# Kernel tuning notes

Measured on AMD Instinct MI355X. Metric: run time of the kernel, lower is better.

The kernel has to match this reference:

```python
import jax, jax.numpy as jnp
import numpy as np

B, N = 2, 6
C_IN, C_MID = 512, 512
D, C_OUT = 112, 80
OGH, OGW, DS = 256, 704, 16
FH, FW = OGH // DS, OGW // DS  # 16, 44
D_MIN, D_MAX = 2.0, 58.0
NX, NY, NZ = 128, 128, 1
VSIZE = np.array([0.8, 0.8, 8.0], dtype=np.float32)
VCOORD = np.array([-51.2 + 0.4, -51.2 + 0.4, -5.0 + 4.0], dtype=np.float32)


def make_frustum():
    # (D, FH, FW, 4) with entries (x_pix, y_pix, depth, 1)
    ones = jnp.ones((D, FH, FW), jnp.float32)
    d = jnp.linspace(D_MIN, D_MAX, D)[:, None, None] * jnp.ones((1, FH, FW))
    x = jnp.linspace(0.0, OGW - 1.0, FW)[None, None, :] * jnp.ones((D, FH, 1))
    y = jnp.linspace(0.0, OGH - 1.0, FH)[None, :, None] * jnp.ones((D, 1, FW))
    return jnp.stack([x, y, d, ones], axis=-1)


def setup_inputs() -> dict:
    key = jax.random.key(0)
    ks = jax.random.split(key, 24)
    eye = jnp.eye(4, dtype=jnp.float32)
    K = jnp.array([[1266.0, 0.0, 800.0, 0.0],
                   [0.0, 1266.0, 450.0, 0.0],
                   [0.0, 0.0, 1.0, 0.0],
                   [0.0, 0.0, 0.0, 1.0]], jnp.float32)
    inp = {
        'feat': jax.random.normal(ks[0], (B * N, C_IN, FH, FW), jnp.float32),
        'w1': 0.05 * jax.random.normal(ks[1], (C_MID, C_IN, 3, 3), jnp.float32),
        'g1': 1.0 + 0.1 * jax.random.normal(ks[2], (C_MID,), jnp.float32),
        'b1': 0.1 * jax.random.normal(ks[3], (C_MID,), jnp.float32),
        'm1': 0.1 * jax.random.normal(ks[4], (C_MID,), jnp.float32),
        'v1': 0.5 + jax.random.uniform(ks[5], (C_MID,), jnp.float32),
        'w2': 0.05 * jax.random.normal(ks[6], (C_MID, C_MID, 3, 3), jnp.float32),
        'g2': 1.0 + 0.1 * jax.random.normal(ks[7], (C_MID,), jnp.float32),
        'b2': 0.1 * jax.random.normal(ks[8], (C_MID,), jnp.float32),
        'm2': 0.1 * jax.random.normal(ks[9], (C_MID,), jnp.float32),
        'v2': 0.5 + jax.random.uniform(ks[10], (C_MID,), jnp.float32),
        'w_out': 0.05 * jax.random.normal(ks[11], (D + C_OUT, C_MID, 1, 1), jnp.float32),
        'b_out': 0.1 * jax.random.normal(ks[12], (D + C_OUT,), jnp.float32),
        'sensor2ego': eye + 0.05 * jax.random.normal(ks[13], (B, N, 4, 4), jnp.float32),
        'sensor2virtual': eye + 0.05 * jax.random.normal(ks[14], (B, N, 4, 4), jnp.float32),
        'intrin': K + 0.01 * jax.random.normal(ks[15], (B, N, 4, 4), jnp.float32),
        'ida': eye + 0.01 * jax.random.normal(ks[16], (B, N, 4, 4), jnp.float32),
        'ref_heights': 1.5 + 0.2 * jax.random.normal(ks[17], (B, N), jnp.float32),
        'bda': eye + 0.01 * jax.random.normal(ks[18], (B, 4, 4), jnp.float32),
    }
    return inp


def _conv(x, w, p):
    return jax.lax.conv_general_dilated(x, w, (1, 1), [(p, p), (p, p)],
                                         dimension_numbers=('NCHW', 'OIHW', 'NCHW'))


def _bn(x, g, b, m, v):
    s = (g / jnp.sqrt(v + 1e-5))
    return (x - m[None, :, None, None]) * s[None, :, None, None] + b[None, :, None, None]


def get_geometry(sensor2ego, sensor2virtual, intrin, ida, ref_heights, bda):
    frustum = make_frustum()[..., None]  # (D,FH,FW,4,1)
    pts = jnp.linalg.inv(ida)[:, :, None, None, None] @ frustum  # (B,N,D,FH,FW,4,1)
    ref = ref_heights[:, :, None, None, None, None]
    height = -pts[..., 2, :] + ref  # (B,N,D,FH,FW,1)
    pc = pts.at[..., 2, :].set(10.0)
    pc = jnp.concatenate([pc[..., :2, :] * pc[..., 2:3, :], pc[..., 2:, :]], axis=-2)
    cv = sensor2virtual @ jnp.linalg.inv(intrin)
    pv = cv[:, :, None, None, None] @ pc
    ratio = height[..., 0] / pv[..., 1, 0]  # (B,N,D,FH,FW)
    pts = pv * ratio[..., None, None]
    pts = pts.at[..., 3, :].set(1.0)
    ce = sensor2ego @ jnp.linalg.inv(sensor2virtual)
    pts = ce[:, :, None, None, None] @ pts
    pts = (bda[:, None, None, None, None] @ pts)[..., 0]
    return pts[..., :3]  # (B,N,D,FH,FW,3)


def reference(feat, w1, g1, b1, m1, v1, w2, g2, b2, m2, v2, w_out, b_out,
              sensor2ego, sensor2virtual, intrin, ida, ref_heights, bda):
    # DepthNet head
    h = jax.nn.relu(_bn(_conv(feat, w1, 1), g1, b1, m1, v1))
    h = jax.nn.relu(_bn(_conv(h, w2, 1), g2, b2, m2, v2))
    hf = _conv(h, w_out, 0) + b_out[None, :, None, None]  # (B*N, D+C, FH, FW)
    depth = jax.nn.softmax(hf[:, :D], axis=1).reshape(B, N, D, FH, FW)
    context = hf[:, D:].reshape(B, N, C_OUT, FH, FW)

    geom = get_geometry(sensor2ego, sensor2virtual, intrin, ida, ref_heights, bda)

    # voxel indices
    vsize = jnp.asarray(VSIZE)
    vcoord = jnp.asarray(VCOORD)
    idx = ((geom - (vcoord - vsize / 2.0)) / vsize).astype(jnp.int32)
    valid = (jnp.all(idx >= 0, axis=-1) & (idx[..., 0] < NX)
             & (idx[..., 1] < NY) & (idx[..., 2] < NZ))

    # LSS outer product: (B,N,D,FH,FW,C)
    vol = jnp.einsum('bndhw,bnchw->bndhwc', depth, context)
    YX = NY * NX
    sid = idx[..., 1] * NX + idx[..., 0] + jnp.arange(B, dtype=jnp.int32)[:, None, None, None, None] * YX
    sid = jnp.where(valid, sid, B * YX).reshape(-1)
    bev = jax.ops.segment_sum(vol.reshape(-1, C_OUT), sid, num_segments=B * YX + 1)[:B * YX]
    return bev.reshape(B, NY, NX, C_OUT).transpose(0, 3, 1, 2)  # (B,C,NY,NX)
```

## Files before the change

### kernel.cpp

```cpp
#include <hip/hip_runtime.h>
#include <stdint.h>

#define NB   2
#define NN   6
#define NIMG 12
#define CIN  512
#define CMID 512
#define DD   112
#define COUT 80
#define FHh  16
#define FWw  44
#define NPIX 704
#define NPOS 8448
#define KK   4608
#define NXg  128
#define NYg  128
#define YX   16384
#define MAT_STRIDE 56
#define PADPIX 828
#define PROW 46
#define KSPLIT 4
#define KCHUNK (KK/KSPLIT)

typedef short short8 __attribute__((ext_vector_type(8)));
typedef float f32x4  __attribute__((ext_vector_type(4)));

#define GLD16(g, l) __builtin_amdgcn_global_load_lds((const __attribute__((address_space(1))) void*)(g), (__attribute__((address_space(3))) void*)(l), 16, 0, 0)

__device__ __forceinline__ unsigned short f2bf(float f){
  unsigned u = __float_as_uint(f);
  u += 0x7fffu + ((u >> 16) & 1u);
  return (unsigned short)(u >> 16);
}

__device__ __forceinline__ f32x4 mfma16(short8 a, short8 b, f32x4 c){
  return __builtin_amdgcn_mfma_f32_16x16x32_bf16(a, b, c, 0, 0, 0);
}

__global__ void k_f32_to_bf16(const float* __restrict__ src, unsigned short* __restrict__ dst, int n){
  for (int i = blockIdx.x*blockDim.x + threadIdx.x; i < n; i += gridDim.x*blockDim.x)
    dst[i] = f2bf(src[i]);
}

__global__ void k_wreorder(const float* __restrict__ src, unsigned short* __restrict__ dst){
  int i = blockIdx.x*blockDim.x + threadIdx.x;
  int oc = i / KK; int j = i - oc*KK;
  int r = j >> 9; int ic = j & 511;
  dst[i] = f2bf(src[(size_t)(oc*512 + ic)*9 + r]);
}

__global__ void k_bn_prep(const float* __restrict__ g, const float* __restrict__ b,
                          const float* __restrict__ m, const float* __restrict__ v,
                          float* __restrict__ scale, float* __restrict__ bias){
  int t = blockIdx.x*blockDim.x + threadIdx.x;
  if (t < CMID){
    float s = g[t] / sqrtf(v[t] + 1e-5f);
    scale[t] = s;
    bias[t]  = b[t] - m[t]*s;
  }
}

__global__ void k_featpad(const float* __restrict__ feat, unsigned short* __restrict__ dst){
  int blk = blockIdx.x;
  int img = blk >> 4, y = blk & 15;
  const float* s = feat + (size_t)img*CIN*NPIX + y*FWw;
  unsigned short* d = dst + (size_t)img*PADPIX*512 + ((y+1)*PROW + 1)*512;
  for (int j = threadIdx.x; j < FWw*512; j += 256){
    int x = j >> 9, ic = j & 511;
    d[x*512 + ic] = f2bf(s[(size_t)ic*NPIX + x]);
  }
}

__device__ void inv4(const double* A, double* out){
  double M[4][8];
  for (int i=0;i<4;i++){ for(int j=0;j<4;j++){ M[i][j]=A[i*4+j]; M[i][4+j]=(i==j)?1.0:0.0; } }
  for (int c=0;c<4;c++){
    int piv=c; double best=fabs(M[c][c]);
    for (int r=c+1;r<4;r++){ double a=fabs(M[r][c]); if(a>best){best=a;piv=r;} }
    if (piv!=c){ for(int j=0;j<8;j++){ double tt=M[c][j]; M[c][j]=M[piv][j]; M[piv][j]=tt; } }
    double inv = 1.0 / M[c][c];
    for (int j=0;j<8;j++) M[c][j]*=inv;
    for (int r=0;r<4;r++){ if(r==c) continue; double f=M[r][c];
      for (int j=0;j<8;j++) M[r][j]-=f*M[c][j]; }
  }
  for (int i=0;i<4;i++) for(int j=0;j<4;j++) out[i*4+j]=M[i][4+j];
}
__device__ void mm4(const double* A, const double* Bm, double* C){
  for (int i=0;i<4;i++) for(int j=0;j<4;j++){
    double s=0.0; for(int k=0;k<4;k++) s+=A[i*4+k]*Bm[k*4+j]; C[i*4+j]=s; }
}

__global__ void k_prep_mats(const float* __restrict__ s2e, const float* __restrict__ s2v,
                            const float* __restrict__ intr, const float* __restrict__ ida,
                            const float* __restrict__ refh, const float* __restrict__ bda,
                            double* __restrict__ mats){
  int t = threadIdx.x;
  if (t >= NIMG) return;
  int b = t / NN;
  double Mida[16], Ms2v[16], Mintr[16], Ms2e[16], Mbda[16];
  for (int i=0;i<16;i++){
    Mida[i] =(double)ida [t*16+i];
    Ms2v[i] =(double)s2v [t*16+i];
    Mintr[i]=(double)intr[t*16+i];
    Ms2e[i] =(double)s2e [t*16+i];
    Mbda[i] =(double)bda [b*16+i];
  }
  double* o = mats + (size_t)t*MAT_STRIDE;
  double tmp[16], tmp2[16];
  inv4(Mida, o);
  inv4(Mintr, tmp);  mm4(Ms2v, tmp, o+16);
  inv4(Ms2v, tmp);   mm4(Ms2e, tmp, tmp2);
  mm4(Mbda, tmp2, o+32);
  o[48] = (double)refh[t];
}

__global__ void k_geom(const double* __restrict__ mats, int* __restrict__ sid){
  int g = blockIdx.x*blockDim.x + threadIdx.x;
  int img = g / (DD*NPIX); int rem = g - img*(DD*NPIX);
  int d = rem / NPIX; int p = rem - d*NPIX;
  int h = p / FWw; int w = p - h*FWw;
  const double* M = mats + (size_t)img*MAT_STRIDE;
  float xf = (float)w * (703.0f/43.0f);
  float yf = (float)h * 17.0f;
  float df = 2.0f + (float)d * (56.0f/111.0f);
  double x = (double)xf, y = (double)yf, dep = (double)df;
  double p0 = M[0]*x + M[1]*y + M[2]*dep + M[3];
  double p1 = M[4]*x + M[5]*y + M[6]*dep + M[7];
  double p2 = M[8]*x + M[9]*y + M[10]*dep + M[11];
  double p3 = M[12]*x + M[13]*y + M[14]*dep + M[15];
  double height = M[48] - p2;
  double c0 = p0*10.0, c1 = p1*10.0, c2 = 10.0, c3 = p3;
  const double* C = M + 16;
  double q0 = C[0]*c0 + C[1]*c1 + C[2]*c2 + C[3]*c3;
  double q1 = C[4]*c0 + C[5]*c1 + C[6]*c2 + C[7]*c3;
  double q2 = C[8]*c0 + C[9]*c1 + C[10]*c2 + C[11]*c3;
  double ratio = height / q1;
  double r0 = q0*ratio, r1 = q1*ratio, r2 = q2*ratio, r3 = 1.0;
  const double* F = M + 32;
  double gx = F[0]*r0 + F[1]*r1 + F[2]*r2 + F[3]*r3;
  double gy = F[4]*r0 + F[5]*r1 + F[6]*r2 + F[7]*r3;
  double gz = F[8]*r0 + F[9]*r1 + F[10]*r2 + F[11]*r3;
  float gxf = (float)gx, gyf = (float)gy, gzf = (float)gz;
  const float vcx = (float)(-51.2 + 0.4);
  const float ox = vcx - 0.4f;
  const float oy = ox;
  const float oz = -1.0f - 4.0f;
  float tx = (gxf - ox) / 0.8f;
  float ty = (gyf - oy) / 0.8f;
  float tz = (gzf - oz) / 8.0f;
  int ix = (int)tx, iy = (int)ty, iz = (int)tz;
  bool valid = (tx==tx) && (ty==ty) && (tz==tz) &&
               (ix >= 0) && (ix < NXg) && (iy >= 0) && (iy < NYg) && (iz == 0);
  int b = img / NN;
  sid[g] = valid ? (b*YX + iy*NXg + ix) : -1;
}

__global__ __launch_bounds__(256, 4) void k_conv_sk(const unsigned short* __restrict__ W,
    const unsigned short* __restrict__ src, float* __restrict__ part){
  __shared__ __align__(16) short As[128*32];
  __shared__ __align__(16) short Bs[128*32];
  int t = threadIdx.x;
  int lane = t & 63, wv = t >> 6;
  int wm = wv >> 1, wn = wv & 1;
  int q = lane >> 4, ml = lane & 15;
  int m0 = blockIdx.x * 128;
  int n0 = blockIdx.y * 128;
  int k0 = blockIdx.z * KCHUNK;

  int lrow = lane >> 2;
  int lcol = (lane & 3) * 8;
  const unsigned short* agp[2];
  const unsigned short* bgp[2];
  #pragma unroll
  for (int i=0;i<2;i++){
    int seg = wv*2 + i;
    agp[i] = W + (size_t)(m0 + seg*16 + lrow)*KK + lcol;
    int pos = n0 + seg*16 + lrow;
    int img = pos / NPIX; int p = pos - img*NPIX;
    int y = p / FWw; int x = p - y*FWw;
    bgp[i] = src + (size_t)img*PADPIX*512 + ((y+1)*PROW + (x+1))*512 + lcol;
  }

  f32x4 acc[4][4];
  #pragma unroll
  for (int i=0;i<4;i++)
    #pragma unroll
    for (int j=0;j<4;j++) acc[i][j] = (f32x4)0.0f;

  for (int kb = k0; kb < k0 + KCHUNK; kb += 32){
    int r = kb >> 9;
    int ic0 = kb & 511;
    int r3 = r / 3;
    int koff = (r3*PROW + (r - r3*3))*512 + ic0 - (PROW+1)*512;
    #pragma unroll
    for (int i=0;i<2;i++){
      int seg = wv*2 + i;
      GLD16(agp[i] + kb,   (char*)As + seg*1024);
      GLD16(bgp[i] + koff, (char*)Bs + seg*1024);
    }
    __syncthreads();
    short8 fa[4], fb[4];
    #pragma unroll
    for (int mi=0;mi<4;mi++) fa[mi] = *(const short8*)(As + (wm*64 + mi*16 + ml)*32 + q*8);
    #pragma unroll
    for (int ni=0;ni<4;ni++) fb[ni] = *(const short8*)(Bs + (wn*64 + ni*16 + ml)*32 + q*8);
    #pragma unroll
    for (int mi=0;mi<4;mi++)
      #pragma unroll
      for (int ni=0;ni<4;ni++)
        acc[mi][ni] = mfma16(fb[ni], fa[mi], acc[mi][ni]);
    __syncthreads();
  }

  float* op = part + (size_t)blockIdx.z*NPOS*CMID;
  #pragma unroll
  for (int mi=0;mi<4;mi++){
    int oc = m0 + wm*64 + mi*16 + ml;
    #pragma unroll
    for (int ni=0;ni<4;ni++){
      f32x4 v = acc[mi][ni];
      #pragma unroll
      for (int rr=0;rr<4;rr++){
        int pos = n0 + wn*64 + ni*16 + q*4 + rr;
        op[(size_t)pos*CMID + oc] = v[rr];
      }
    }
  }
}

template<int OUT_PADDED>
__global__ void k_reduce(const float* __restrict__ part,
                         const float* __restrict__ scale, const float* __restrict__ bias,
                         unsigned short* __restrict__ out){
  int i = blockIdx.x*blockDim.x + threadIdx.x;
  int pos = i >> 9, oc = i & 511;
  const size_t S = (size_t)NPOS*CMID;
  float sum = part[i] + part[i + S] + part[i + 2*S] + part[i + 3*S];
  float val = fmaxf(sum*scale[oc] + bias[oc], 0.0f);
  unsigned short bv = f2bf(val);
  if (OUT_PADDED){
    int img = pos / NPIX; int p = pos - img*NPIX;
    int y = p / FWw; int x = p - y*FWw;
    out[(size_t)img*PADPIX*512 + ((y+1)*PROW + (x+1))*512 + oc] = bv;
  } else {
    out[i] = bv;
  }
}

__global__ __launch_bounds__(256) void k_gemm64(const unsigned short* __restrict__ A,
    const unsigned short* __restrict__ Bt, const float* __restrict__ bout,
    float* __restrict__ hf){
  const int K = 512;
  __shared__ __align__(16) short As[64][32];
  __shared__ __align__(16) short Bs[128][32];
  int t = threadIdx.x;
  int m0 = blockIdx.x*64; int n0 = blockIdx.y*128;
  int lane = t & 63; int wv = t >> 6; int q = lane >> 4, ml = lane & 15;
  f32x4 acc[8];
  #pragma unroll
  for (int i=0;i<8;i++) acc[i] = (f32x4)0.0f;
  int ar = t >> 2, ac = (t & 3) * 8;
  int br = t >> 1, bc = (t & 1) * 16;
  const unsigned short* pa = A  + (size_t)(m0 + ar)*K + ac;
  const unsigned short* pb = Bt + (size_t)(n0 + br)*K + bc;
  for (int kb = 0; kb < K; kb += 32){
    uint4 av = *(const uint4*)(pa + kb);
    uint4 b0 = *(const uint4*)(pb + kb);
    uint4 b1 = *(const uint4*)(pb + kb + 8);
    __syncthreads();
    *(uint4*)&As[ar][ac] = av;
    *(uint4*)&Bs[br][bc] = b0; *(uint4*)&Bs[br][bc+8] = b1;
    __syncthreads();
    short8 fa = *(const short8*)&As[wv*16 + ml][q*8];
    #pragma unroll
    for (int ni=0;ni<8;ni++){
      short8 fb = *(const short8*)&Bs[ni*16 + ml][q*8];
      acc[ni] = mfma16(fb, fa, acc[ni]);
    }
  }
  int oc = m0 + wv*16 + ml;
  float bb = bout[oc];
  #pragma unroll
  for (int ni=0;ni<8;ni++)
    #pragma unroll
    for (int r=0;r<4;r++){
      int pos = n0 + ni*16 + q*4 + r;
      hf[(size_t)pos*192 + oc] = acc[ni][r] + bb;
    }
}

__global__ void k_softmax(const float* __restrict__ hf, float* __restrict__ depth){
  int pos = blockIdx.x*4 + (threadIdx.x >> 6);
  int lane = threadIdx.x & 63;
  const float* row = hf + (size_t)pos*192;
  float v0 = row[lane];
  float v1 = (lane < DD-64) ? row[64 + lane] : -1e30f;
  float mx = fmaxf(v0, v1);
  #pragma unroll
  for (int m=1; m<64; m<<=1) mx = fmaxf(mx, __shfl_xor(mx, m, 64));
  float e0 = expf(v0 - mx);
  float e1 = (lane < DD-64) ? expf(v1 - mx) : 0.0f;
  float s = e0 + e1;
  #pragma unroll
  for (int m=1; m<64; m<<=1) s += __shfl_xor(s, m, 64);
  float inv = 1.0f / s;
  depth[(size_t)pos*DD + lane] = e0 * inv;
  if (lane < DD-64) depth[(size_t)pos*DD + 64 + lane] = e1 * inv;
}

__global__ void k_scatter(const float* __restrict__ depth, const float* __restrict__ hf,
                          const int* __restrict__ sidb, float* __restrict__ bev){
  int pos = blockIdx.x;
  int img = pos / NPIX; int p = pos - img*NPIX;
  __shared__ float sdep[DD];
  __shared__ int   ssid[DD];
  __shared__ float sctx[COUT];
  __shared__ float cwt[DD];
  __shared__ int   cvox[DD];
  __shared__ int   scnt;
  int t = threadIdx.x;
  if (t == 0) scnt = 0;
  if (t < DD){
    sdep[t] = depth[(size_t)pos*DD + t];
    ssid[t] = sidb[(size_t)(img*DD + t)*NPIX + p];
  }
  if (t < COUT) sctx[t] = hf[(size_t)pos*192 + DD + t];
  __syncthreads();
  if (t < DD){
    int s = ssid[t];
    bool head = (s >= 0) && (t == 0 || ssid[t-1] != s);
    if (head){
      float w = 0.0f;
      for (int dd = t; dd < DD && ssid[dd] == s; ++dd) w += sdep[dd];
      int i = atomicAdd(&scnt, 1);
      cvox[i] = s; cwt[i] = w;
    }
  }
  __syncthreads();
  int H = scnt;
  for (int j = t; j < H*COUT; j += 128){
    int h = j / COUT, c = j - h*COUT;
    atomicAdd(&bev[(size_t)cvox[h]*COUT + c], cwt[h]*sctx[c]);
  }
}

__global__ void k_transpose(const float* __restrict__ bev, float* __restrict__ out){
  int i = blockIdx.x*blockDim.x + threadIdx.x;
  int yx = i & (YX-1); int rest = i >> 14;
  int c = rest % COUT; int b = rest / COUT;
  out[i] = bev[((size_t)(b*YX + yx))*COUT + c];
}

extern "C" void kernel_launch(void* const* d_in, const int* in_sizes, int n_in,
                              void* d_out, int out_size, void* d_ws, size_t ws_size,
                              hipStream_t stream) {
  const float* feat = (const float*)d_in[0];
  const float* w1   = (const float*)d_in[1];
  const float* g1   = (const float*)d_in[2];
  const float* b1   = (const float*)d_in[3];
  const float* m1   = (const float*)d_in[4];
  const float* v1   = (const float*)d_in[5];
  const float* w2   = (const float*)d_in[6];
  const float* g2   = (const float*)d_in[7];
  const float* b2   = (const float*)d_in[8];
  const float* m2   = (const float*)d_in[9];
  const float* v2   = (const float*)d_in[10];
  const float* wout = (const float*)d_in[11];
  const float* bout = (const float*)d_in[12];
  const float* s2e  = (const float*)d_in[13];
  const float* s2v  = (const float*)d_in[14];
  const float* intr = (const float*)d_in[15];
  const float* ida  = (const float*)d_in[16];
  const float* refh = (const float*)d_in[17];
  const float* bda  = (const float*)d_in[18];

  uint8_t* base = (uint8_t*)d_ws;
  size_t off = 0;
  auto alloc = [&](size_t bytes)->void*{
    void* r = base + off;
    off = (off + bytes + 255) & ~(size_t)255;
    return r;
  };
  unsigned short* wb1 = (unsigned short*)alloc((size_t)CMID*KK*2);
  unsigned short* wb2 = (unsigned short*)alloc((size_t)CMID*KK*2);
  unsigned short* wb3 = (unsigned short*)alloc((size_t)192*CMID*2);
  float* scale1 = (float*)alloc(CMID*4);
  float* bias1  = (float*)alloc(CMID*4);
  float* scale2 = (float*)alloc(CMID*4);
  float* bias2  = (float*)alloc(CMID*4);
  double* mats  = (double*)alloc((size_t)NIMG*MAT_STRIDE*8);

  size_t padded_bytes = (size_t)NIMG*PADPIX*512*2;
  uint8_t* regionE = (uint8_t*)alloc(padded_bytes);
  uint8_t* regionF = (uint8_t*)alloc(padded_bytes);
  float* depth = (float*)alloc((size_t)NPOS*DD*4);
  int*   sid   = (int*)  alloc((size_t)NIMG*DD*NPIX*4);
  float* bev   = (float*)alloc((size_t)NB*YX*COUT*4);
  float* part  = (float*)alloc((size_t)KSPLIT*NPOS*CMID*4);

  unsigned short* featpad = (unsigned short*)regionE;
  unsigned short* h2      = (unsigned short*)regionE;
  unsigned short* h1pad   = (unsigned short*)regionF;
  float*          hf      = (float*)regionF;

  k_wreorder<<<9216, 256, 0, stream>>>(w1, wb1);
  k_wreorder<<<9216, 256, 0, stream>>>(w2, wb2);
  k_f32_to_bf16<<<384, 256, 0, stream>>>(wout, wb3, 192*CMID);
  k_bn_prep<<<2, 256, 0, stream>>>(g1, b1, m1, v1, scale1, bias1);
  k_bn_prep<<<2, 256, 0, stream>>>(g2, b2, m2, v2, scale2, bias2);
  k_prep_mats<<<1, 64, 0, stream>>>(s2e, s2v, intr, ida, refh, bda, mats);
  k_geom<<<3696, 256, 0, stream>>>(mats, sid);

  hipMemsetAsync(featpad, 0, padded_bytes, stream);
  hipMemsetAsync(h1pad,   0, padded_bytes, stream);
  k_featpad<<<192, 256, 0, stream>>>(feat, featpad);

  k_conv_sk<<<dim3(4, 66, KSPLIT), 256, 0, stream>>>(wb1, featpad, part);
  k_reduce<1><<<16896, 256, 0, stream>>>(part, scale1, bias1, h1pad);
  k_conv_sk<<<dim3(4, 66, KSPLIT), 256, 0, stream>>>(wb2, h1pad, part);
  k_reduce<0><<<16896, 256, 0, stream>>>(part, scale2, bias2, h2);
  k_gemm64<<<dim3(3, 66), 256, 0, stream>>>(wb3, h2, bout, hf);

  k_softmax<<<2112, 256, 0, stream>>>(hf, depth);

  hipMemsetAsync(bev, 0, (size_t)NB*YX*COUT*4, stream);
  k_scatter<<<NPOS, 128, 0, stream>>>(depth, hf, sid, bev);

  k_transpose<<<10240, 256, 0, stream>>>(bev, (float*)d_out);
}
```

Before: 424.0 us.

## Store split-K partials in bf16, fuse prep kernels, border-only zeroing, tiled transpose

Several independent changes. The split-K conv partial sums are written as bf16 instead of fp32, which halves partial-buffer traffic, and the reduce kernel now handles two channels per thread. The five weight and BN prep kernels are merged into one launch. The two full-buffer memsets are replaced by a kernel that zeroes only the padding border. The final transpose stages data through shared memory for coalesced access. Rounding each partial sum to bf16 before accumulation adds numerical error.

```diff
diff --git a/kernel.cpp b/kernel.cpp
--- a/kernel.cpp
+++ b/kernel.cpp
@@ -32,32 +32,57 @@
   u += 0x7fffu + ((u >> 16) & 1u);
   return (unsigned short)(u >> 16);
 }
+__device__ __forceinline__ float bf2f(unsigned short u){
+  return __uint_as_float(((unsigned)u) << 16);
+}
 
 __device__ __forceinline__ f32x4 mfma16(short8 a, short8 b, f32x4 c){
   return __builtin_amdgcn_mfma_f32_16x16x32_bf16(a, b, c, 0, 0, 0);
 }
 
-__global__ void k_f32_to_bf16(const float* __restrict__ src, unsigned short* __restrict__ dst, int n){
-  for (int i = blockIdx.x*blockDim.x + threadIdx.x; i < n; i += gridDim.x*blockDim.x)
-    dst[i] = f2bf(src[i]);
-}
-
-__global__ void k_wreorder(const float* __restrict__ src, unsigned short* __restrict__ dst){
+#define N1 (CMID*KK)
+__global__ void k_prep_misc(const float* __restrict__ w1, const float* __restrict__ w2,
+                            const float* __restrict__ wout,
+                            const float* __restrict__ g1, const float* __restrict__ b1,
+                            const float* __restrict__ m1, const float* __restrict__ v1,
+                            const float* __restrict__ g2, const float* __restrict__ b2,
+                            const float* __restrict__ m2, const float* __restrict__ v2,
+                            unsigned short* __restrict__ wb1, unsigned short* __restrict__ wb2,
+                            unsigned short* __restrict__ wb3,
+                            float* __restrict__ scale1, float* __restrict__ bias1,
+                            float* __restrict__ scale2, float* __restrict__ bias2){
   int i = blockIdx.x*blockDim.x + threadIdx.x;
-  int oc = i / KK; int j = i - oc*KK;
-  int r = j >> 9; int ic = j & 511;
-  dst[i] = f2bf(src[(size_t)(oc*512 + ic)*9 + r]);
-}
-
-__global__ void k_bn_prep(const float* __restrict__ g, const float* __restrict__ b,
-                          const float* __restrict__ m, const float* __restrict__ v,
-                          float* __restrict__ scale, float* __restrict__ bias){
-  int t = blockIdx.x*blockDim.x + threadIdx.x;
-  if (t < CMID){
-    float s = g[t] / sqrtf(v[t] + 1e-5f);
-    scale[t] = s;
-    bias[t]  = b[t] - m[t]*s;
-  }
+  if (i < 2*N1){
+    const float* w = (i < N1) ? w1 : w2;
+    unsigned short* wb = (i < N1) ? wb1 : wb2;
+    int j = (i < N1) ? i : i - N1;
+    int oc = j / KK; int jj = j - oc*KK;
+    int r = jj >> 9; int ic = jj & 511;
+    wb[j] = f2bf(w[(size_t)(oc*512 + ic)*9 + r]);
+  } else if (i < 2*N1 + 192*CMID){
+    int j = i - 2*N1;
+    wb3[j] = f2bf(wout[j]);
+  } else if (i < 2*N1 + 192*CMID + 512){
+    int t = i - (2*N1 + 192*CMID);
+    float s = g1[t] / sqrtf(v1[t] + 1e-5f);
+    scale1[t] = s; bias1[t] = b1[t] - m1[t]*s;
+  } else if (i < 2*N1 + 192*CMID + 1024){
+    int t = i - (2*N1 + 192*CMID + 512);
+    float s = g2[t] / sqrtf(v2[t] + 1e-5f);
+    scale2[t] = s; bias2[t] = b2[t] - m2[t]*s;
+  }
+}
+
+__global__ void k_zeropad(unsigned short* __restrict__ a, unsigned short* __restrict__ b){
+  int i = blockIdx.x*blockDim.x + threadIdx.x;
+  int img = i >> 16; int j = i & 65535;
+  int seg = j >> 9, ch = j & 511;
+  int pp;
+  if (seg < 46)       pp = seg;
+  else if (seg < 92)  pp = 17*PROW + (seg - 46);
+  else { int s2 = seg - 92; int y = s2 >> 1; pp = y*PROW + ((s2 & 1) ? 45 : 0); }
+  size_t off = (size_t)img*PADPIX*512 + (size_t)pp*512 + ch;
+  a[off] = 0; b[off] = 0;
 }
 
 __global__ void k_featpad(const float* __restrict__ feat, unsigned short* __restrict__ dst){
@@ -156,7 +181,7 @@
 }
 
 __global__ __launch_bounds__(256, 4) void k_conv_sk(const unsigned short* __restrict__ W,
-    const unsigned short* __restrict__ src, float* __restrict__ part){
+    const unsigned short* __restrict__ src, unsigned short* __restrict__ part){
   __shared__ __align__(16) short As[128*32];
   __shared__ __align__(16) short Bs[128*32];
   int t = threadIdx.x;
@@ -212,7 +237,7 @@
     __syncthreads();
   }
 
-  float* op = part + (size_t)blockIdx.z*NPOS*CMID;
+  unsigned short* op = part + (size_t)blockIdx.z*NPOS*CMID;
   #pragma unroll
   for (int mi=0;mi<4;mi++){
     int oc = m0 + wm*64 + mi*16 + ml;
@@ -222,28 +247,37 @@
       #pragma unroll
       for (int rr=0;rr<4;rr++){
         int pos = n0 + wn*64 + ni*16 + q*4 + rr;
-        op[(size_t)pos*CMID + oc] = v[rr];
+        op[(size_t)pos*CMID + oc] = f2bf(v[rr]);
       }
     }
   }
 }
 
 template<int OUT_PADDED>
-__global__ void k_reduce(const float* __restrict__ part,
+__global__ void k_reduce(const unsigned short* __restrict__ part,
                          const float* __restrict__ scale, const float* __restrict__ bias,
                          unsigned short* __restrict__ out){
-  int i = blockIdx.x*blockDim.x + threadIdx.x;
-  int pos = i >> 9, oc = i & 511;
+  int i2 = blockIdx.x*blockDim.x + threadIdx.x;
+  int e0 = i2*2;
   const size_t S = (size_t)NPOS*CMID;
-  float sum = part[i] + part[i + S] + part[i + 2*S] + part[i + 3*S];
-  float val = fmaxf(sum*scale[oc] + bias[oc], 0.0f);
-  unsigned short bv = f2bf(val);
+  unsigned p0 = *(const unsigned*)(part + e0);
+  unsigned p1 = *(const unsigned*)(part + e0 + S);
+  unsigned p2 = *(const unsigned*)(part + e0 + 2*S);
+  unsigned p3 = *(const unsigned*)(part + e0 + 3*S);
+  float s0 = bf2f((unsigned short)p0) + bf2f((unsigned short)p1)
+           + bf2f((unsigned short)p2) + bf2f((unsigned short)p3);
+  float s1 = bf2f((unsigned short)(p0>>16)) + bf2f((unsigned short)(p1>>16))
+           + bf2f((unsigned short)(p2>>16)) + bf2f((unsigned short)(p3>>16));
+  int pos = e0 >> 9, oc = e0 & 511;
+  float v0 = fmaxf(s0*scale[oc]   + bias[oc],   0.0f);
+  float v1 = fmaxf(s1*scale[oc+1] + bias[oc+1], 0.0f);
+  unsigned packed = (unsigned)f2bf(v0) | ((unsigned)f2bf(v1) << 16);
   if (OUT_PADDED){
     int img = pos / NPIX; int p = pos - img*NPIX;
     int y = p / FWw; int x = p - y*FWw;
-    out[(size_t)img*PADPIX*512 + ((y+1)*PROW + (x+1))*512 + oc] = bv;
+    *(unsigned*)(out + (size_t)img*PADPIX*512 + ((y+1)*PROW + (x+1))*512 + oc) = packed;
   } else {
-    out[i] = bv;
+    *(unsigned*)(out + e0) = packed;
   }
 }
 
@@ -344,11 +378,19 @@
   }
 }
 
-__global__ void k_transpose(const float* __restrict__ bev, float* __restrict__ out){
-  int i = blockIdx.x*blockDim.x + threadIdx.x;
-  int yx = i & (YX-1); int rest = i >> 14;
-  int c = rest % COUT; int b = rest / COUT;
-  out[i] = bev[((size_t)(b*YX + yx))*COUT + c];
+__global__ __launch_bounds__(256) void k_transpose(const float* __restrict__ bev, float* __restrict__ out){
+  __shared__ float tile[64*COUT];
+  int blk = blockIdx.x;
+  int b = blk >> 8; int yx0 = (blk & 255) * 64;
+  int t = threadIdx.x;
+  const float* src = bev + ((size_t)b*YX + yx0)*COUT;
+  for (int j = t; j < 64*COUT; j += 256) tile[j] = src[j];
+  __syncthreads();
+  float* dst = out + (size_t)b*COUT*YX + yx0;
+  for (int j = t; j < COUT*64; j += 256){
+    int c = j >> 6, row = j & 63;
+    dst[(size_t)c*YX + row] = tile[row*COUT + c];
+  }
 }
 
 extern "C" void kernel_launch(void* const* d_in, const int* in_sizes, int n_in,
@@ -396,29 +438,26 @@
   float* depth = (float*)alloc((size_t)NPOS*DD*4);
   int*   sid   = (int*)  alloc((size_t)NIMG*DD*NPIX*4);
   float* bev   = (float*)alloc((size_t)NB*YX*COUT*4);
-  float* part  = (float*)alloc((size_t)KSPLIT*NPOS*CMID*4);
+  unsigned short* part = (unsigned short*)alloc((size_t)KSPLIT*NPOS*CMID*2);
 
   unsigned short* featpad = (unsigned short*)regionE;
   unsigned short* h2      = (unsigned short*)regionE;
   unsigned short* h1pad   = (unsigned short*)regionF;
   float*          hf      = (float*)regionF;
 
-  k_wreorder<<<9216, 256, 0, stream>>>(w1, wb1);
-  k_wreorder<<<9216, 256, 0, stream>>>(w2, wb2);
-  k_f32_to_bf16<<<384, 256, 0, stream>>>(wout, wb3, 192*CMID);
-  k_bn_prep<<<2, 256, 0, stream>>>(g1, b1, m1, v1, scale1, bias1);
-  k_bn_prep<<<2, 256, 0, stream>>>(g2, b2, m2, v2, scale2, bias2);
+  int prep_n = 2*N1 + 192*CMID + 1024;
+  k_prep_misc<<<(prep_n + 255)/256, 256, 0, stream>>>(w1, w2, wout, g1, b1, m1, v1,
+      g2, b2, m2, v2, wb1, wb2, wb3, scale1, bias1, scale2, bias2);
   k_prep_mats<<<1, 64, 0, stream>>>(s2e, s2v, intr, ida, refh, bda, mats);
   k_geom<<<3696, 256, 0, stream>>>(mats, sid);
 
-  hipMemsetAsync(featpad, 0, padded_bytes, stream);
-  hipMemsetAsync(h1pad,   0, padded_bytes, stream);
+  k_zeropad<<<3072, 256, 0, stream>>>(featpad, h1pad);
   k_featpad<<<192, 256, 0, stream>>>(feat, featpad);
 
   k_conv_sk<<<dim3(4, 66, KSPLIT), 256, 0, stream>>>(wb1, featpad, part);
-  k_reduce<1><<<16896, 256, 0, stream>>>(part, scale1, bias1, h1pad);
+  k_reduce<1><<<NPOS*CMID/512, 256, 0, stream>>>(part, scale1, bias1, h1pad);
   k_conv_sk<<<dim3(4, 66, KSPLIT), 256, 0, stream>>>(wb2, h1pad, part);
-  k_reduce<0><<<16896, 256, 0, stream>>>(part, scale2, bias2, h2);
+  k_reduce<0><<<NPOS*CMID/512, 256, 0, stream>>>(part, scale2, bias2, h2);
   k_gemm64<<<dim3(3, 66), 256, 0, stream>>>(wb3, h2, bout, hf);
 
   k_softmax<<<2112, 256, 0, stream>>>(hf, depth);
@@ -426,5 +465,5 @@
   hipMemsetAsync(bev, 0, (size_t)NB*YX*COUT*4, stream);
   k_scatter<<<NPOS, 128, 0, stream>>>(depth, hf, sid, bev);
 
-  k_transpose<<<10240, 256, 0, stream>>>(bev, (float*)d_out);
-}
+  k_transpose<<<512, 256, 0, stream>>>(bev, (float*)d_out);
+}
```

Result: faster. 394.8 us (-6.9%).
